# Kernel tuning notes

Hardware: AMD Instinct MI355X
Metric: run time of the kernel (lower is better)

The kernel has to match this reference:

```python
import jax, jax.numpy as jnp
import numpy as np

NZ = 1024       # opts.nz (== NH so layer-0 input weights stack with other layers)
NH = 1024       # opts.nh
NSTATE = 64     # opts.n_state
NLAYERS = 4
MAX_PRIM_LEN = 100
T = MAX_PRIM_LEN + 1   # max_unroll=True runs exactly max_prim_len+1 steps
P_BIAS = 1.0           # opts.dec_p_bias


def setup_inputs() -> dict:
    key = jax.random.key(0)
    ks = jax.random.split(key, 9)
    s_ih = 1.0 / np.sqrt(NH)
    u = lambda k, shape: jax.random.uniform(k, shape, jnp.float32, -s_ih, s_ih)
    return {
        "z": jax.random.normal(ks[0], (1, NZ), jnp.float32),
        # torch LSTM params, gate order (i, f, g, o); layer0 input dim == NZ == NH
        "Wih": u(ks[1], (NLAYERS, 4 * NH, NH)),
        "Whh": u(ks[2], (NLAYERS, 4 * NH, NH)),
        "bih": u(ks[3], (NLAYERS, 4 * NH)),
        "bhh": u(ks[4], (NLAYERS, 4 * NH)),
        "Ws": u(ks[5], (NSTATE, NH)),
        "bs": u(ks[6], (NSTATE,)),
        "Wp": u(ks[7], (2, NH)),
        "bp": u(ks[8], (2,)),
    }


def reference(z, Wih, Whh, bih, bhh, Ws, bs, Wp, bp):
    z0 = z.reshape(-1)  # (NZ,)
    zeros = jnp.zeros_like(z0)

    def step(carry, i):
        h, c = carry                      # each (NLAYERS, NH)
        x = jnp.where(i == 0, z0, zeros)  # input is z at t=0, zeros after
        hs, cs = [], []
        inp = x
        for l in range(NLAYERS):
            gates = Wih[l] @ inp + bih[l] + Whh[l] @ h[l] + bhh[l]
            gi, gf, gg, go = jnp.split(gates, 4)
            cl = jax.nn.sigmoid(gf) * c[l] + jax.nn.sigmoid(gi) * jnp.tanh(gg)
            hl = jax.nn.sigmoid(go) * jnp.tanh(cl)
            hs.append(hl)
            cs.append(cl)
            inp = hl
        o = inp                            # top-layer output, (NH,)
        s = Ws @ o + bs                    # state head, (NSTATE,)
        logits = (Wp @ o + bp).at[0].add(P_BIAS)
        p = jax.nn.softmax(logits)         # (2,)
        last = i == T - 1                  # torch: t > max_prim_len -> force [0,1]
        p = jnp.where(last, jnp.array([0.0, 1.0], p.dtype), p)
        samp = jnp.where(last, 1, 0).astype(jnp.int64)  # max_unroll forces 0 until last
        return (jnp.stack(hs), jnp.stack(cs)), (s, p, samp)

    h0 = jnp.zeros((NLAYERS, NH), z.dtype)
    _, (states, probs, samples) = jax.lax.scan(step, (h0, h0), jnp.arange(T))
    return states[:, None, :], probs[:, None, :], samples[:, None]
```

## Files before the change

### kernel.cpp

```cpp
#include <hip/hip_runtime.h>


#define TT    101
#define NBLK  256
#define NTH   512
#define NREP  8
#define SLAB_U32 512
#define HB16_BYTES (4 * TT * NREP * SLAB_U32 * 4)
#define OUT_PROBS 6464
#define OUT_SAMP  6666
#define SENT 0xFFFFFFFFu

typedef _Float16 h2 __attribute__((ext_vector_type(2)));

__device__ __forceinline__ h2 mkh2(float a, float b) {
    h2 r; r.x = (_Float16)a; r.y = (_Float16)b; return r;
}
__device__ __forceinline__ unsigned pack2(float a, float b) {
    return __builtin_bit_cast(unsigned, mkh2(a, b));
}
__device__ __forceinline__ h2 as_h2(unsigned u) { return __builtin_bit_cast(h2, u); }

#if __has_builtin(__builtin_amdgcn_fdot2)
__device__ __forceinline__ float fdot2(h2 a, h2 b, float c) {
    return __builtin_amdgcn_fdot2(a, b, c, false);
}
#else
__device__ __forceinline__ float fdot2(h2 a, h2 b, float c) {
    return fmaf((float)a.x, (float)b.x, fmaf((float)a.y, (float)b.y, c));
}
#endif

__device__ __forceinline__ uint4 load16_bypass(const uint4* p) {
    uint4 r;
    asm volatile("global_load_dwordx4 %0, %1, off sc0 sc1\n\ts_waitcnt vmcnt(0)"
                 : "=v"(r) : "v"(p) : "memory");
    return r;
}
__device__ __forceinline__ void store4_bypass(unsigned* p, unsigned v) {
    asm volatile("global_store_dword %0, %1, off sc0 sc1" :: "v"(p), "v"(v) : "memory");
}
__device__ __forceinline__ uint4 poll16(const uint4* p) {
    uint4 r = load16_bypass(p);
    while (r.x == SENT || r.y == SENT || r.z == SENT || r.w == SENT) {
        __builtin_amdgcn_s_sleep(1);
        r = load16_bypass(p);
    }
    return r;
}

__device__ __forceinline__ float wave_sum(float x) {
    int v;
    v = __builtin_amdgcn_update_dpp(0, __builtin_bit_cast(int, x), 0x111, 0xf, 0xf, false);
    x += __builtin_bit_cast(float, v);
    v = __builtin_amdgcn_update_dpp(0, __builtin_bit_cast(int, x), 0x112, 0xf, 0xf, false);
    x += __builtin_bit_cast(float, v);
    v = __builtin_amdgcn_update_dpp(0, __builtin_bit_cast(int, x), 0x114, 0xf, 0xe, false);
    x += __builtin_bit_cast(float, v);
    v = __builtin_amdgcn_update_dpp(0, __builtin_bit_cast(int, x), 0x118, 0xf, 0xc, false);
    x += __builtin_bit_cast(float, v);
    v = __builtin_amdgcn_update_dpp(0, __builtin_bit_cast(int, x), 0x142, 0xa, 0xf, false);
    x += __builtin_bit_cast(float, v);
    v = __builtin_amdgcn_update_dpp(0, __builtin_bit_cast(int, x), 0x143, 0xc, 0xf, false);
    x += __builtin_bit_cast(float, v);
    return __builtin_bit_cast(float, __builtin_amdgcn_readlane(__builtin_bit_cast(int, x), 63));
}

__device__ __forceinline__ float sigm(float x) { return 1.f / (1.f + expf(-x)); }

__global__ __launch_bounds__(NTH, 2) void lstm_kernel(
    const float* __restrict__ z,
    const float* __restrict__ Wih, const float* __restrict__ Whh,
    const float* __restrict__ bih, const float* __restrict__ bhh,
    const float* __restrict__ Ws,  const float* __restrict__ bs,
    const float* __restrict__ Wp,  const float* __restrict__ bp,
    unsigned* __restrict__ hb16, float* __restrict__ out)
{
    const int tid  = threadIdx.x;
    const int wv   = tid >> 6;
    const int lane = tid & 63;
    const int l    = blockIdx.x >> 6;
    const int gb   = blockIdx.x & 63;
    const int uA   = (gb << 4) + (wv << 1);

    __shared__ __align__(16) uint4 vh4[256];
    __shared__ unsigned hout[8];

    h2 w[8][16];
    #pragma unroll
    for (int r = 0; r < 8; ++r) {
        const int u = uA + (r >> 2);
        const int g = r & 3;
        const size_t row = ((size_t)((l << 12) + (g << 10) + u)) << 10;
        const float4* pa = (const float4*)(Whh + row + (lane << 3));
        const float4* pb = (const float4*)(Whh + row + 512 + (lane << 3));
        const float4* pc = (const float4*)(Wih + row + (lane << 3));
        const float4* pd = (const float4*)(Wih + row + 512 + (lane << 3));
        float4 f;
        f = pa[0]; w[r][0]  = mkh2(f.x, f.y); w[r][1]  = mkh2(f.z, f.w);
        f = pa[1]; w[r][2]  = mkh2(f.x, f.y); w[r][3]  = mkh2(f.z, f.w);
        f = pb[0]; w[r][4]  = mkh2(f.x, f.y); w[r][5]  = mkh2(f.z, f.w);
        f = pb[1]; w[r][6]  = mkh2(f.x, f.y); w[r][7]  = mkh2(f.z, f.w);
        f = pc[0]; w[r][8]  = mkh2(f.x, f.y); w[r][9]  = mkh2(f.z, f.w);
        f = pc[1]; w[r][10] = mkh2(f.x, f.y); w[r][11] = mkh2(f.z, f.w);
        f = pd[0]; w[r][12] = mkh2(f.x, f.y); w[r][13] = mkh2(f.z, f.w);
        f = pd[1]; w[r][14] = mkh2(f.x, f.y); w[r][15] = mkh2(f.z, f.w);
    }

    float bA[4], bB[4];
    #pragma unroll
    for (int g = 0; g < 4; ++g) {
        const int iA = (l << 12) + (g << 10) + uA;
        bA[g] = bih[iA] + bhh[iA];
        bB[g] = bih[iA + 1] + bhh[iA + 1];
    }

    const bool role_states = (l == 0 && wv == 6);
    const bool role_probs  = (l == 1 && gb == 0 && wv == 6);
    float hw0[16], hw1[16], hb0 = 0.f, hb1 = 0.f;
    if (role_states) {
        #pragma unroll
        for (int k = 0; k < 16; ++k) hw0[k] = Ws[(gb << 10) + (lane << 4) + k];
        hb0 = bs[gb];
    } else if (role_probs) {
        #pragma unroll
        for (int k = 0; k < 16; ++k) {
            hw0[k] = Wp[(lane << 4) + k];
            hw1[k] = Wp[1024 + (lane << 4) + k];
        }
        hb0 = bp[0]; hb1 = bp[1];
    }
    int th = 0;

    float cstA = 0.f, cstB = 0.f;

    #pragma unroll 1
    for (int t = 0; t < TT; ++t) {
        const bool full = (l > 0) || (t == 0);
        const int rep = (gb + wv) & (NREP - 1);

        if (wv < 2) {
            const int c = (wv << 6) + lane;
            if (t == 0) vh4[c] = make_uint4(0, 0, 0, 0);
            else {
                const uint4* slab = (const uint4*)(hb16 + (size_t)((l * TT + t - 1) * NREP + rep) * SLAB_U32);
                vh4[c] = poll16(slab + c);
            }
        } else if (wv < 4) {
            const int c = ((wv - 2) << 6) + lane;
            if (l > 0) {
                const uint4* slab = (const uint4*)(hb16 + (size_t)(((l - 1) * TT + t) * NREP + rep) * SLAB_U32);
                vh4[128 + c] = poll16(slab + c);
            } else if (t == 0) {
                const float4 f0 = *(const float4*)(z + (c << 3));
                const float4 f1 = *(const float4*)(z + (c << 3) + 4);
                vh4[128 + c] = make_uint4(pack2(f0.x, f0.y), pack2(f0.z, f0.w),
                                          pack2(f1.x, f1.y), pack2(f1.z, f1.w));
            }
        }
        __syncthreads();

        float acc[8] = {0.f, 0.f, 0.f, 0.f, 0.f, 0.f, 0.f, 0.f};
        {
            const uint4 A1 = vh4[lane];
            const uint4 A2 = vh4[64 + lane];
            const unsigned a8[8] = {A1.x, A1.y, A1.z, A1.w, A2.x, A2.y, A2.z, A2.w};
            #pragma unroll
            for (int k = 0; k < 8; ++k) {
                const h2 v2 = as_h2(a8[k]);
                #pragma unroll
                for (int r = 0; r < 8; ++r) acc[r] = fdot2(w[r][k], v2, acc[r]);
            }
            if (full) {
                const uint4 B1 = vh4[128 + lane];
                const uint4 B2 = vh4[192 + lane];
                const unsigned b8[8] = {B1.x, B1.y, B1.z, B1.w, B2.x, B2.y, B2.z, B2.w};
                #pragma unroll
                for (int k = 0; k < 8; ++k) {
                    const h2 v2 = as_h2(b8[k]);
                    #pragma unroll
                    for (int r = 0; r < 8; ++r) acc[r] = fdot2(w[r][8 + k], v2, acc[r]);
                }
            }
        }

        float tot[8];
        #pragma unroll
        for (int r = 0; r < 8; ++r) tot[r] = wave_sum(acc[r]);

        cstA = fmaf(sigm(tot[1] + bA[1]), cstA, sigm(tot[0] + bA[0]) * tanhf(tot[2] + bA[2]));
        cstB = fmaf(sigm(tot[5] + bB[1]), cstB, sigm(tot[4] + bB[0]) * tanhf(tot[6] + bB[2]));
        const float hA = sigm(tot[3] + bA[3]) * tanhf(cstA);
        const float hB = sigm(tot[7] + bB[3]) * tanhf(cstB);
        if (lane == 0) hout[wv] = pack2(hA, hB);
        __syncthreads();

        if (wv == 7) {
            const unsigned val = hout[lane & 7];
            unsigned* addr = hb16 + (size_t)(l * TT + t) * NREP * SLAB_U32
                           + (size_t)(lane >> 3) * SLAB_U32 + (gb << 3) + (lane & 7);
            store4_bypass(addr, val);
        } else if ((role_states || role_probs) && th < TT && th <= t - 3) {
            const int hrep = (gb + th) & (NREP - 1);
            const uint4* slab3 = (const uint4*)(hb16 + (size_t)((3 * TT + th) * NREP + hrep) * SLAB_U32);
            const uint4 r0 = load16_bypass(slab3 + (lane << 1));
            const uint4 r1 = load16_bypass(slab3 + (lane << 1) + 1);
            const bool ok = !(r0.x == SENT || r0.y == SENT || r0.z == SENT || r0.w == SENT ||
                              r1.x == SENT || r1.y == SENT || r1.z == SENT || r1.w == SENT);
            if (__ballot(ok) == ~0ull) {
                const unsigned u8[8] = {r0.x, r0.y, r0.z, r0.w, r1.x, r1.y, r1.z, r1.w};
                if (role_states) {
                    float a = 0.f;
                    #pragma unroll
                    for (int j = 0; j < 8; ++j) {
                        const h2 p = as_h2(u8[j]);
                        a = fmaf(hw0[2 * j], (float)p.x, a);
                        a = fmaf(hw0[2 * j + 1], (float)p.y, a);
                    }
                    const float tots = wave_sum(a);
                    if (lane == 0) out[th * 64 + gb] = tots + hb0;
                } else {
                    float a0 = 0.f, a1 = 0.f;
                    #pragma unroll
                    for (int j = 0; j < 8; ++j) {
                        const h2 p = as_h2(u8[j]);
                        a0 = fmaf(hw0[2 * j], (float)p.x, a0); a0 = fmaf(hw0[2 * j + 1], (float)p.y, a0);
                        a1 = fmaf(hw1[2 * j], (float)p.x, a1); a1 = fmaf(hw1[2 * j + 1], (float)p.y, a1);
                    }
                    const float t0 = wave_sum(a0), t1 = wave_sum(a1);
                    if (lane == 0) {
                        float p0, p1;
                        if (th == TT - 1) { p0 = 0.f; p1 = 1.f; }
                        else {
                            const float l0 = t0 + hb0 + 1.0f;
                            const float l1 = t1 + hb1;
                            const float m  = fmaxf(l0, l1);
                            const float e0 = expf(l0 - m), e1 = expf(l1 - m);
                            const float inv = 1.f / (e0 + e1);
                            p0 = e0 * inv; p1 = e1 * inv;
                        }
                        out[OUT_PROBS + 2 * th]     = p0;
                        out[OUT_PROBS + 2 * th + 1] = p1;
                        out[OUT_SAMP + th] = (th == TT - 1) ? 1.0f : 0.0f;
                    }
                }
                ++th;
            }
        }
    }

    if (role_states || role_probs) {
        while (th < TT) {
            const int hrep = (gb + th) & (NREP - 1);
            const uint4* slab3 = (const uint4*)(hb16 + (size_t)((3 * TT + th) * NREP + hrep) * SLAB_U32);
            const uint4 r0 = poll16(slab3 + (lane << 1));
            const uint4 r1 = poll16(slab3 + (lane << 1) + 1);
            const unsigned u8[8] = {r0.x, r0.y, r0.z, r0.w, r1.x, r1.y, r1.z, r1.w};
            if (role_states) {
                float a = 0.f;
                #pragma unroll
                for (int j = 0; j < 8; ++j) {
                    const h2 p = as_h2(u8[j]);
                    a = fmaf(hw0[2 * j], (float)p.x, a);
                    a = fmaf(hw0[2 * j + 1], (float)p.y, a);
                }
                const float tots = wave_sum(a);
                if (lane == 0) out[th * 64 + gb] = tots + hb0;
            } else {
                float a0 = 0.f, a1 = 0.f;
                #pragma unroll
                for (int j = 0; j < 8; ++j) {
                    const h2 p = as_h2(u8[j]);
                    a0 = fmaf(hw0[2 * j], (float)p.x, a0); a0 = fmaf(hw0[2 * j + 1], (float)p.y, a0);
                    a1 = fmaf(hw1[2 * j], (float)p.x, a1); a1 = fmaf(hw1[2 * j + 1], (float)p.y, a1);
                }
                const float t0 = wave_sum(a0), t1 = wave_sum(a1);
                if (lane == 0) {
                    float p0, p1;
                    if (th == TT - 1) { p0 = 0.f; p1 = 1.f; }
                    else {
                        const float l0 = t0 + hb0 + 1.0f;
                        const float l1 = t1 + hb1;
                        const float m  = fmaxf(l0, l1);
                        const float e0 = expf(l0 - m), e1 = expf(l1 - m);
                        const float inv = 1.f / (e0 + e1);
                        p0 = e0 * inv; p1 = e1 * inv;
                    }
                    out[OUT_PROBS + 2 * th]     = p0;
                    out[OUT_PROBS + 2 * th + 1] = p1;
                    out[OUT_SAMP + th] = (th == TT - 1) ? 1.0f : 0.0f;
                }
            }
            ++th;
        }
    }
}

extern "C" void kernel_launch(void* const* d_in, const int* in_sizes, int n_in,
                              void* d_out, int out_size, void* d_ws, size_t ws_size,
                              hipStream_t stream)
{
    const float* z   = (const float*)d_in[0];
    const float* Wih = (const float*)d_in[1];
    const float* Whh = (const float*)d_in[2];
    const float* bih = (const float*)d_in[3];
    const float* bhh = (const float*)d_in[4];
    const float* Ws  = (const float*)d_in[5];
    const float* bs  = (const float*)d_in[6];
    const float* Wp  = (const float*)d_in[7];
    const float* bp  = (const float*)d_in[8];
    float* out = (float*)d_out;

    unsigned* hb16 = (unsigned*)d_ws;

    hipMemsetAsync(hb16, 0xFF, HB16_BYTES, stream);
    lstm_kernel<<<NBLK, NTH, 0, stream>>>(z, Wih, Whh, bih, bhh,
                                          Ws, bs, Wp, bp, hb16, out);
}
```

Measured before the change: 506.2 us.

## Double-buffer LDS vectors, pipeline polling, replace barrier with LDS flag handoff

Double-buffers the shared hidden-state vectors so waves 0-3 fetch the next step's inputs right after the current step's compute, which drops one __syncthreads per step. Wave 7 now waits on sentinel-flagged LDS slots instead of a barrier. Polling uses a hand-written asm loop that keeps two sets of per-dword loads in flight and retires lanes as they complete. Fast __expf-based sigmoid/tanh and paired loads for the head reads are added. The LDS spin handoff and the fast math add correctness and precision risk.

Measured after the change: 573.7 us. 13.3% more time.

```diff
diff --git a/kernel.cpp b/kernel.cpp
--- a/kernel.cpp
+++ b/kernel.cpp
@@ -31,22 +31,88 @@
 }
 #endif
 
-__device__ __forceinline__ uint4 load16_bypass(const uint4* p) {
-    uint4 r;
-    asm volatile("global_load_dwordx4 %0, %1, off sc0 sc1\n\ts_waitcnt vmcnt(0)"
-                 : "=v"(r) : "v"(p) : "memory");
-    return r;
-}
 __device__ __forceinline__ void store4_bypass(unsigned* p, unsigned v) {
     asm volatile("global_store_dword %0, %1, off sc0 sc1" :: "v"(p), "v"(v) : "memory");
 }
-__device__ __forceinline__ uint4 poll16(const uint4* p) {
-    uint4 r = load16_bypass(p);
-    while (r.x == SENT || r.y == SENT || r.z == SENT || r.w == SENT) {
-        __builtin_amdgcn_s_sleep(1);
-        r = load16_bypass(p);
-    }
-    return r;
+
+__device__ __forceinline__ void load32_bypass2(const uint4* p0, const uint4* p1,
+                                               uint4& r0, uint4& r1) {
+    asm volatile("global_load_dwordx4 %0, %2, off sc0 sc1\n\t"
+                 "global_load_dwordx4 %1, %3, off sc0 sc1\n\t"
+                 "s_waitcnt vmcnt(0)"
+                 : "=&v"(r0), "=&v"(r1) : "v"(p0), "v"(p1) : "memory");
+}
+
+__device__ __forceinline__ uint4 poll16_pipe(const uint4* p) {
+    unsigned r0, r1, r2, r3, a0, a1, a2, a3, b0, b1, b2, b3;
+    unsigned long long se, sm, st;
+    asm volatile(
+        "s_mov_b64 %12, exec\n\t"
+        "global_load_dword %4, %15, off sc0 sc1\n\t"
+        "global_load_dword %5, %15, off offset:4 sc0 sc1\n\t"
+        "global_load_dword %6, %15, off offset:8 sc0 sc1\n\t"
+        "global_load_dword %7, %15, off offset:12 sc0 sc1\n\t"
+        "s_sleep 8\n\t"
+        "global_load_dword %8, %15, off sc0 sc1\n\t"
+        "global_load_dword %9, %15, off offset:4 sc0 sc1\n\t"
+        "global_load_dword %10, %15, off offset:8 sc0 sc1\n\t"
+        "global_load_dword %11, %15, off offset:12 sc0 sc1\n\t"
+        "Lploop%=:\n\t"
+        "s_waitcnt vmcnt(4)\n\t"
+        "v_cmp_ne_u32 vcc, -1, %4\n\t"
+        "s_mov_b64 %13, vcc\n\t"
+        "v_cmp_ne_u32 vcc, -1, %5\n\t"
+        "s_and_b64 %13, %13, vcc\n\t"
+        "v_cmp_ne_u32 vcc, -1, %6\n\t"
+        "s_and_b64 %13, %13, vcc\n\t"
+        "v_cmp_ne_u32 vcc, -1, %7\n\t"
+        "s_and_b64 %13, %13, vcc\n\t"
+        "s_mov_b64 %14, exec\n\t"
+        "s_mov_b64 exec, %13\n\t"
+        "v_mov_b32 %0, %4\n\t"
+        "v_mov_b32 %1, %5\n\t"
+        "v_mov_b32 %2, %6\n\t"
+        "v_mov_b32 %3, %7\n\t"
+        "s_mov_b64 exec, %14\n\t"
+        "s_andn2_b64 exec, exec, %13\n\t"
+        "s_cbranch_execz Lpdone%=\n\t"
+        "global_load_dword %4, %15, off sc0 sc1\n\t"
+        "global_load_dword %5, %15, off offset:4 sc0 sc1\n\t"
+        "global_load_dword %6, %15, off offset:8 sc0 sc1\n\t"
+        "global_load_dword %7, %15, off offset:12 sc0 sc1\n\t"
+        "s_waitcnt vmcnt(4)\n\t"
+        "v_cmp_ne_u32 vcc, -1, %8\n\t"
+        "s_mov_b64 %13, vcc\n\t"
+        "v_cmp_ne_u32 vcc, -1, %9\n\t"
+        "s_and_b64 %13, %13, vcc\n\t"
+        "v_cmp_ne_u32 vcc, -1, %10\n\t"
+        "s_and_b64 %13, %13, vcc\n\t"
+        "v_cmp_ne_u32 vcc, -1, %11\n\t"
+        "s_and_b64 %13, %13, vcc\n\t"
+        "s_mov_b64 %14, exec\n\t"
+        "s_mov_b64 exec, %13\n\t"
+        "v_mov_b32 %0, %8\n\t"
+        "v_mov_b32 %1, %9\n\t"
+        "v_mov_b32 %2, %10\n\t"
+        "v_mov_b32 %3, %11\n\t"
+        "s_mov_b64 exec, %14\n\t"
+        "s_andn2_b64 exec, exec, %13\n\t"
+        "s_cbranch_execz Lpdone%=\n\t"
+        "global_load_dword %8, %15, off sc0 sc1\n\t"
+        "global_load_dword %9, %15, off offset:4 sc0 sc1\n\t"
+        "global_load_dword %10, %15, off offset:8 sc0 sc1\n\t"
+        "global_load_dword %11, %15, off offset:12 sc0 sc1\n\t"
+        "s_branch Lploop%=\n\t"
+        "Lpdone%=:\n\t"
+        "s_mov_b64 exec, %12\n\t"
+        "s_waitcnt vmcnt(0)"
+        : "=&v"(r0), "=&v"(r1), "=&v"(r2), "=&v"(r3),
+          "=&v"(a0), "=&v"(a1), "=&v"(a2), "=&v"(a3),
+          "=&v"(b0), "=&v"(b1), "=&v"(b2), "=&v"(b3),
+          "=&s"(se), "=&s"(sm), "=&s"(st)
+        : "v"(p)
+        : "vcc", "scc", "memory");
+    return make_uint4(r0, r1, r2, r3);
 }
 
 __device__ __forceinline__ float wave_sum(float x) {
@@ -66,7 +132,8 @@
     return __builtin_bit_cast(float, __builtin_amdgcn_readlane(__builtin_bit_cast(int, x), 63));
 }
 
-__device__ __forceinline__ float sigm(float x) { return 1.f / (1.f + expf(-x)); }
+__device__ __forceinline__ float sigm(float x)   { return 1.f / (1.f + __expf(-x)); }
+__device__ __forceinline__ float tanh_f(float x) { return 1.f - 2.f / (1.f + __expf(x + x)); }
 
 __global__ __launch_bounds__(NTH, 2) void lstm_kernel(
     const float* __restrict__ z,
@@ -83,7 +150,7 @@
     const int gb   = blockIdx.x & 63;
     const int uA   = (gb << 4) + (wv << 1);
 
-    __shared__ __align__(16) uint4 vh4[256];
+    __shared__ __align__(16) uint4 vh4[2][256];
     __shared__ unsigned hout[8];
 
     h2 w[8][16];
@@ -134,36 +201,34 @@
 
     float cstA = 0.f, cstB = 0.f;
 
+    if (tid < 8) hout[tid] = SENT;
+    if (wv < 2) {
+        const int c = (wv << 6) + lane;
+        vh4[0][c] = make_uint4(0, 0, 0, 0);
+    } else if (wv < 4) {
+        const int c = ((wv - 2) << 6) + lane;
+        if (l == 0) {
+            const float4 f0 = *(const float4*)(z + (c << 3));
+            const float4 f1 = *(const float4*)(z + (c << 3) + 4);
+            vh4[0][128 + c] = make_uint4(pack2(f0.x, f0.y), pack2(f0.z, f0.w),
+                                         pack2(f1.x, f1.y), pack2(f1.z, f1.w));
+        } else {
+            const int rep = (gb + wv) & (NREP - 1);
+            const uint4* slab = (const uint4*)(hb16 + (size_t)(((l - 1) * TT) * NREP + rep) * SLAB_U32);
+            vh4[0][128 + c] = poll16_pipe(slab + c);
+        }
+    }
+    __syncthreads();
+
     #pragma unroll 1
     for (int t = 0; t < TT; ++t) {
         const bool full = (l > 0) || (t == 0);
-        const int rep = (gb + wv) & (NREP - 1);
-
-        if (wv < 2) {
-            const int c = (wv << 6) + lane;
-            if (t == 0) vh4[c] = make_uint4(0, 0, 0, 0);
-            else {
-                const uint4* slab = (const uint4*)(hb16 + (size_t)((l * TT + t - 1) * NREP + rep) * SLAB_U32);
-                vh4[c] = poll16(slab + c);
-            }
-        } else if (wv < 4) {
-            const int c = ((wv - 2) << 6) + lane;
-            if (l > 0) {
-                const uint4* slab = (const uint4*)(hb16 + (size_t)(((l - 1) * TT + t) * NREP + rep) * SLAB_U32);
-                vh4[128 + c] = poll16(slab + c);
-            } else if (t == 0) {
-                const float4 f0 = *(const float4*)(z + (c << 3));
-                const float4 f1 = *(const float4*)(z + (c << 3) + 4);
-                vh4[128 + c] = make_uint4(pack2(f0.x, f0.y), pack2(f0.z, f0.w),
-                                          pack2(f1.x, f1.y), pack2(f1.z, f1.w));
-            }
-        }
-        __syncthreads();
+        const int rb = t & 1;
 
         float acc[8] = {0.f, 0.f, 0.f, 0.f, 0.f, 0.f, 0.f, 0.f};
         {
-            const uint4 A1 = vh4[lane];
-            const uint4 A2 = vh4[64 + lane];
+            const uint4 A1 = vh4[rb][lane];
+            const uint4 A2 = vh4[rb][64 + lane];
             const unsigned a8[8] = {A1.x, A1.y, A1.z, A1.w, A2.x, A2.y, A2.z, A2.w};
             #pragma unroll
             for (int k = 0; k < 8; ++k) {
@@ -172,8 +237,8 @@
                 for (int r = 0; r < 8; ++r) acc[r] = fdot2(w[r][k], v2, acc[r]);
             }
             if (full) {
-                const uint4 B1 = vh4[128 + lane];
-                const uint4 B2 = vh4[192 + lane];
+                const uint4 B1 = vh4[rb][128 + lane];
+                const uint4 B2 = vh4[rb][192 + lane];
                 const unsigned b8[8] = {B1.x, B1.y, B1.z, B1.w, B2.x, B2.y, B2.z, B2.w};
                 #pragma unroll
                 for (int k = 0; k < 8; ++k) {
@@ -188,23 +253,39 @@
         #pragma unroll
         for (int r = 0; r < 8; ++r) tot[r] = wave_sum(acc[r]);
 
-        cstA = fmaf(sigm(tot[1] + bA[1]), cstA, sigm(tot[0] + bA[0]) * tanhf(tot[2] + bA[2]));
-        cstB = fmaf(sigm(tot[5] + bB[1]), cstB, sigm(tot[4] + bB[0]) * tanhf(tot[6] + bB[2]));
-        const float hA = sigm(tot[3] + bA[3]) * tanhf(cstA);
-        const float hB = sigm(tot[7] + bB[3]) * tanhf(cstB);
-        if (lane == 0) hout[wv] = pack2(hA, hB);
-        __syncthreads();
+        cstA = fmaf(sigm(tot[1] + bA[1]), cstA, sigm(tot[0] + bA[0]) * tanh_f(tot[2] + bA[2]));
+        cstB = fmaf(sigm(tot[5] + bB[1]), cstB, sigm(tot[4] + bB[0]) * tanh_f(tot[6] + bB[2]));
+        const float hA = sigm(tot[3] + bA[3]) * tanh_f(cstA);
+        const float hB = sigm(tot[7] + bB[3]) * tanh_f(cstB);
+        if (lane == 0) ((volatile unsigned*)hout)[wv] = pack2(hA, hB);
 
         if (wv == 7) {
-            const unsigned val = hout[lane & 7];
+            volatile unsigned* vho = (volatile unsigned*)hout;
+            unsigned v = vho[lane & 7];
+            while (v == SENT) { v = vho[lane & 7]; }
+            if (lane < 8) vho[lane] = SENT;
             unsigned* addr = hb16 + (size_t)(l * TT + t) * NREP * SLAB_U32
                            + (size_t)(lane >> 3) * SLAB_U32 + (gb << 3) + (lane & 7);
-            store4_bypass(addr, val);
+            store4_bypass(addr, v);
+        } else if (wv < 2) {
+            if (t + 1 < TT) {
+                const int c = (wv << 6) + lane;
+                const int rep = (gb + wv) & (NREP - 1);
+                const uint4* slab = (const uint4*)(hb16 + (size_t)((l * TT + t) * NREP + rep) * SLAB_U32);
+                vh4[rb ^ 1][c] = poll16_pipe(slab + c);
+            }
+        } else if (wv < 4) {
+            if (t + 1 < TT && l > 0) {
+                const int c = ((wv - 2) << 6) + lane;
+                const int rep = (gb + wv) & (NREP - 1);
+                const uint4* slab = (const uint4*)(hb16 + (size_t)(((l - 1) * TT + (t + 1)) * NREP + rep) * SLAB_U32);
+                vh4[rb ^ 1][128 + c] = poll16_pipe(slab + c);
+            }
         } else if ((role_states || role_probs) && th < TT && th <= t - 3) {
             const int hrep = (gb + th) & (NREP - 1);
             const uint4* slab3 = (const uint4*)(hb16 + (size_t)((3 * TT + th) * NREP + hrep) * SLAB_U32);
-            const uint4 r0 = load16_bypass(slab3 + (lane << 1));
-            const uint4 r1 = load16_bypass(slab3 + (lane << 1) + 1);
+            uint4 r0, r1;
+            load32_bypass2(slab3 + (lane << 1), slab3 + (lane << 1) + 1, r0, r1);
             const bool ok = !(r0.x == SENT || r0.y == SENT || r0.z == SENT || r0.w == SENT ||
                               r1.x == SENT || r1.y == SENT || r1.z == SENT || r1.w == SENT);
             if (__ballot(ok) == ~0ull) {
@@ -247,14 +328,20 @@
                 ++th;
             }
         }
+        __syncthreads();
     }
 
     if (role_states || role_probs) {
         while (th < TT) {
             const int hrep = (gb + th) & (NREP - 1);
             const uint4* slab3 = (const uint4*)(hb16 + (size_t)((3 * TT + th) * NREP + hrep) * SLAB_U32);
-            const uint4 r0 = poll16(slab3 + (lane << 1));
-            const uint4 r1 = poll16(slab3 + (lane << 1) + 1);
+            uint4 r0, r1;
+            for (;;) {
+                load32_bypass2(slab3 + (lane << 1), slab3 + (lane << 1) + 1, r0, r1);
+                if (!(r0.x == SENT || r0.y == SENT || r0.z == SENT || r0.w == SENT ||
+                      r1.x == SENT || r1.y == SENT || r1.z == SENT || r1.w == SENT)) break;
+                __builtin_amdgcn_s_sleep(1);
+            }
             const unsigned u8[8] = {r0.x, r0.y, r0.z, r0.w, r1.x, r1.y, r1.z, r1.w};
             if (role_states) {
                 float a = 0.f;
```

## Drop shared-memory staging and block barriers; each wave polls its own hidden state

Applied to the files above, without the earlier changes.

Each wave now loads the previous-step and lower-layer hidden-state slabs from global memory straight into registers, and publishes its own packed h values. This removes the LDS staging buffer and both per-step __syncthreads, so waves within a block no longer wait on each other. The A and B slabs are issued as batched bypass loads behind a single wait. sigmoid and tanh switch to __expf-based approximations. The cost is roughly eight times more global and L2 polling traffic per block, and slightly lower transcendental accuracy.

Result: slower. 1.058 ms (+109.0%).

```diff
diff --git a/kernel.cpp b/kernel.cpp
--- a/kernel.cpp
+++ b/kernel.cpp
@@ -31,22 +31,32 @@
 }
 #endif
 
-__device__ __forceinline__ uint4 load16_bypass(const uint4* p) {
-    uint4 r;
-    asm volatile("global_load_dwordx4 %0, %1, off sc0 sc1\n\ts_waitcnt vmcnt(0)"
-                 : "=v"(r) : "v"(p) : "memory");
-    return r;
-}
 __device__ __forceinline__ void store4_bypass(unsigned* p, unsigned v) {
     asm volatile("global_store_dword %0, %1, off sc0 sc1" :: "v"(p), "v"(v) : "memory");
 }
-__device__ __forceinline__ uint4 poll16(const uint4* p) {
-    uint4 r = load16_bypass(p);
-    while (r.x == SENT || r.y == SENT || r.z == SENT || r.w == SENT) {
-        __builtin_amdgcn_s_sleep(1);
-        r = load16_bypass(p);
-    }
-    return r;
+
+__device__ __forceinline__ void load32_bypass2(const uint4* p0, const uint4* p1,
+                                               uint4& r0, uint4& r1) {
+    asm volatile("global_load_dwordx4 %0, %2, off sc0 sc1\n\t"
+                 "global_load_dwordx4 %1, %3, off sc0 sc1\n\t"
+                 "s_waitcnt vmcnt(0)"
+                 : "=&v"(r0), "=&v"(r1) : "v"(p0), "v"(p1) : "memory");
+}
+
+__device__ __forceinline__ void load64_bypass4(const uint4* p0, const uint4* p1,
+                                               const uint4* p2, const uint4* p3,
+                                               uint4& r0, uint4& r1, uint4& r2, uint4& r3) {
+    asm volatile("global_load_dwordx4 %0, %4, off sc0 sc1\n\t"
+                 "global_load_dwordx4 %1, %5, off sc0 sc1\n\t"
+                 "global_load_dwordx4 %2, %6, off sc0 sc1\n\t"
+                 "global_load_dwordx4 %3, %7, off sc0 sc1\n\t"
+                 "s_waitcnt vmcnt(0)"
+                 : "=&v"(r0), "=&v"(r1), "=&v"(r2), "=&v"(r3)
+                 : "v"(p0), "v"(p1), "v"(p2), "v"(p3) : "memory");
+}
+
+__device__ __forceinline__ bool stale(const uint4& u) {
+    return (u.x == SENT) | (u.y == SENT) | (u.z == SENT) | (u.w == SENT);
 }
 
 __device__ __forceinline__ float wave_sum(float x) {
@@ -66,7 +76,8 @@
     return __builtin_bit_cast(float, __builtin_amdgcn_readlane(__builtin_bit_cast(int, x), 63));
 }
 
-__device__ __forceinline__ float sigm(float x) { return 1.f / (1.f + expf(-x)); }
+__device__ __forceinline__ float sigm(float x)   { return 1.f / (1.f + __expf(-x)); }
+__device__ __forceinline__ float tanh_f(float x) { return 1.f - 2.f / (1.f + __expf(x + x)); }
 
 __global__ __launch_bounds__(NTH, 2) void lstm_kernel(
     const float* __restrict__ z,
@@ -82,9 +93,6 @@
     const int l    = blockIdx.x >> 6;
     const int gb   = blockIdx.x & 63;
     const int uA   = (gb << 4) + (wv << 1);
-
-    __shared__ __align__(16) uint4 vh4[256];
-    __shared__ unsigned hout[8];
 
     h2 w[8][16];
     #pragma unroll
@@ -136,34 +144,53 @@
 
     #pragma unroll 1
     for (int t = 0; t < TT; ++t) {
-        const bool full = (l > 0) || (t == 0);
         const int rep = (gb + wv) & (NREP - 1);
-
-        if (wv < 2) {
-            const int c = (wv << 6) + lane;
-            if (t == 0) vh4[c] = make_uint4(0, 0, 0, 0);
-            else {
-                const uint4* slab = (const uint4*)(hb16 + (size_t)((l * TT + t - 1) * NREP + rep) * SLAB_U32);
-                vh4[c] = poll16(slab + c);
-            }
-        } else if (wv < 4) {
-            const int c = ((wv - 2) << 6) + lane;
-            if (l > 0) {
-                const uint4* slab = (const uint4*)(hb16 + (size_t)(((l - 1) * TT + t) * NREP + rep) * SLAB_U32);
-                vh4[128 + c] = poll16(slab + c);
-            } else if (t == 0) {
-                const float4 f0 = *(const float4*)(z + (c << 3));
-                const float4 f1 = *(const float4*)(z + (c << 3) + 4);
-                vh4[128 + c] = make_uint4(pack2(f0.x, f0.y), pack2(f0.z, f0.w),
-                                          pack2(f1.x, f1.y), pack2(f1.z, f1.w));
-            }
-        }
-        __syncthreads();
+        const bool needA = (t > 0);
+        const bool needB = (l > 0);
+        uint4 A1 = {}, A2 = {}, B1 = {}, B2 = {};
+
+        if (needA && needB) {
+            const uint4* pa = (const uint4*)(hb16 + (size_t)((l * TT + t - 1) * NREP + rep) * SLAB_U32);
+            const uint4* pb = (const uint4*)(hb16 + (size_t)(((l - 1) * TT + t) * NREP + rep) * SLAB_U32);
+            load64_bypass4(pa + lane, pa + 64 + lane, pb + lane, pb + 64 + lane,
+                           A1, A2, B1, B2);
+            while (stale(A1) | stale(A2)) {
+                __builtin_amdgcn_s_sleep(1);
+                load32_bypass2(pa + lane, pa + 64 + lane, A1, A2);
+            }
+            while (stale(B1) | stale(B2)) {
+                __builtin_amdgcn_s_sleep(1);
+                load32_bypass2(pb + lane, pb + 64 + lane, B1, B2);
+            }
+        } else if (needA) {
+            const uint4* pa = (const uint4*)(hb16 + (size_t)((l * TT + t - 1) * NREP + rep) * SLAB_U32);
+            load32_bypass2(pa + lane, pa + 64 + lane, A1, A2);
+            while (stale(A1) | stale(A2)) {
+                __builtin_amdgcn_s_sleep(1);
+                load32_bypass2(pa + lane, pa + 64 + lane, A1, A2);
+            }
+        } else if (needB) {
+            const uint4* pb = (const uint4*)(hb16 + (size_t)(((l - 1) * TT) * NREP + rep) * SLAB_U32);
+            load32_bypass2(pb + lane, pb + 64 + lane, B1, B2);
+            while (stale(B1) | stale(B2)) {
+                __builtin_amdgcn_s_sleep(1);
+                load32_bypass2(pb + lane, pb + 64 + lane, B1, B2);
+            }
+        }
+        const bool fullB = needB || (t == 0);
+        if (l == 0 && t == 0) {
+            const float4 f0 = *(const float4*)(z + (lane << 3));
+            const float4 f1 = *(const float4*)(z + (lane << 3) + 4);
+            const float4 f2 = *(const float4*)(z + 512 + (lane << 3));
+            const float4 f3 = *(const float4*)(z + 512 + (lane << 3) + 4);
+            B1 = make_uint4(pack2(f0.x, f0.y), pack2(f0.z, f0.w),
+                            pack2(f1.x, f1.y), pack2(f1.z, f1.w));
+            B2 = make_uint4(pack2(f2.x, f2.y), pack2(f2.z, f2.w),
+                            pack2(f3.x, f3.y), pack2(f3.z, f3.w));
+        }
 
         float acc[8] = {0.f, 0.f, 0.f, 0.f, 0.f, 0.f, 0.f, 0.f};
-        {
-            const uint4 A1 = vh4[lane];
-            const uint4 A2 = vh4[64 + lane];
+        if (needA) {
             const unsigned a8[8] = {A1.x, A1.y, A1.z, A1.w, A2.x, A2.y, A2.z, A2.w};
             #pragma unroll
             for (int k = 0; k < 8; ++k) {
@@ -171,16 +198,14 @@
                 #pragma unroll
                 for (int r = 0; r < 8; ++r) acc[r] = fdot2(w[r][k], v2, acc[r]);
             }
-            if (full) {
-                const uint4 B1 = vh4[128 + lane];
-                const uint4 B2 = vh4[192 + lane];
-                const unsigned b8[8] = {B1.x, B1.y, B1.z, B1.w, B2.x, B2.y, B2.z, B2.w};
+        }
+        if (fullB) {
+            const unsigned b8[8] = {B1.x, B1.y, B1.z, B1.w, B2.x, B2.y, B2.z, B2.w};
+            #pragma unroll
+            for (int k = 0; k < 8; ++k) {
+                const h2 v2 = as_h2(b8[k]);
                 #pragma unroll
-                for (int k = 0; k < 8; ++k) {
-                    const h2 v2 = as_h2(b8[k]);
-                    #pragma unroll
-                    for (int r = 0; r < 8; ++r) acc[r] = fdot2(w[r][8 + k], v2, acc[r]);
-                }
+                for (int r = 0; r < 8; ++r) acc[r] = fdot2(w[r][8 + k], v2, acc[r]);
             }
         }
 
@@ -188,25 +213,24 @@
         #pragma unroll
         for (int r = 0; r < 8; ++r) tot[r] = wave_sum(acc[r]);
 
-        cstA = fmaf(sigm(tot[1] + bA[1]), cstA, sigm(tot[0] + bA[0]) * tanhf(tot[2] + bA[2]));
-        cstB = fmaf(sigm(tot[5] + bB[1]), cstB, sigm(tot[4] + bB[0]) * tanhf(tot[6] + bB[2]));
-        const float hA = sigm(tot[3] + bA[3]) * tanhf(cstA);
-        const float hB = sigm(tot[7] + bB[3]) * tanhf(cstB);
-        if (lane == 0) hout[wv] = pack2(hA, hB);
-        __syncthreads();
-
-        if (wv == 7) {
-            const unsigned val = hout[lane & 7];
-            unsigned* addr = hb16 + (size_t)(l * TT + t) * NREP * SLAB_U32
-                           + (size_t)(lane >> 3) * SLAB_U32 + (gb << 3) + (lane & 7);
+        cstA = fmaf(sigm(tot[1] + bA[1]), cstA, sigm(tot[0] + bA[0]) * tanh_f(tot[2] + bA[2]));
+        cstB = fmaf(sigm(tot[5] + bB[1]), cstB, sigm(tot[4] + bB[0]) * tanh_f(tot[6] + bB[2]));
+        const float hA = sigm(tot[3] + bA[3]) * tanh_f(cstA);
+        const float hB = sigm(tot[7] + bB[3]) * tanh_f(cstB);
+
+        const unsigned val = pack2(hA, hB);
+        if (lane < NREP) {
+            unsigned* addr = hb16 + (size_t)((l * TT + t) * NREP) * SLAB_U32
+                           + (size_t)lane * SLAB_U32 + (gb << 3) + wv;
             store4_bypass(addr, val);
-        } else if ((role_states || role_probs) && th < TT && th <= t - 3) {
+        }
+
+        if ((role_states || role_probs) && th < TT && th <= t - 3) {
             const int hrep = (gb + th) & (NREP - 1);
             const uint4* slab3 = (const uint4*)(hb16 + (size_t)((3 * TT + th) * NREP + hrep) * SLAB_U32);
-            const uint4 r0 = load16_bypass(slab3 + (lane << 1));
-            const uint4 r1 = load16_bypass(slab3 + (lane << 1) + 1);
-            const bool ok = !(r0.x == SENT || r0.y == SENT || r0.z == SENT || r0.w == SENT ||
-                              r1.x == SENT || r1.y == SENT || r1.z == SENT || r1.w == SENT);
+            uint4 r0, r1;
+            load32_bypass2(slab3 + (lane << 1), slab3 + (lane << 1) + 1, r0, r1);
+            const bool ok = !(stale(r0) | stale(r1));
             if (__ballot(ok) == ~0ull) {
                 const unsigned u8[8] = {r0.x, r0.y, r0.z, r0.w, r1.x, r1.y, r1.z, r1.w};
                 if (role_states) {
@@ -253,8 +277,12 @@
         while (th < TT) {
             const int hrep = (gb + th) & (NREP - 1);
             const uint4* slab3 = (const uint4*)(hb16 + (size_t)((3 * TT + th) * NREP + hrep) * SLAB_U32);
-            const uint4 r0 = poll16(slab3 + (lane << 1));
-            const uint4 r1 = poll16(slab3 + (lane << 1) + 1);
+            uint4 r0, r1;
+            for (;;) {
+                load32_bypass2(slab3 + (lane << 1), slab3 + (lane << 1) + 1, r0, r1);
+                if (!(stale(r0) | stale(r1))) break;
+                __builtin_amdgcn_s_sleep(1);
+            }
             const unsigned u8[8] = {r0.x, r0.y, r0.z, r0.w, r1.x, r1.y, r1.z, r1.w};
             if (role_states) {
                 float a = 0.f;
```

## Gate slab polling on per-step arrival counters and use fast exp activations

Applied to the files above, without the earlier changes.

Adds a per-(layer, step) atomic counter that each producer block bumps after storing its h slice. Consumers whose first slab read is stale now spin on that single counter until all 64 producers have arrived, then re-read the slab. This is meant to cut repeated wide polling traffic on the h buffers. The change also merges the paired 16-byte bypass loads into one asm block with a single wait, and swaps expf/tanhf for __expf-based sigmoid and tanh. The fast math loses some accuracy, and the counter path only runs if the workspace is large enough.

Measured after the change: 644.6 us. 1.27x slower.

```diff
diff --git a/kernel.cpp b/kernel.cpp
--- a/kernel.cpp
+++ b/kernel.cpp
@@ -6,7 +6,9 @@
 #define NTH   512
 #define NREP  8
 #define SLAB_U32 512
-#define HB16_BYTES (4 * TT * NREP * SLAB_U32 * 4)
+#define HB16_U32  (4 * TT * NREP * SLAB_U32)
+#define HB16_BYTES (HB16_U32 * 4)
+#define CNT_BYTES (4 * TT * 4)
 #define OUT_PROBS 6464
 #define OUT_SAMP  6666
 #define SENT 0xFFFFFFFFu
@@ -37,14 +39,38 @@
                  : "=v"(r) : "v"(p) : "memory");
     return r;
 }
+__device__ __forceinline__ unsigned load4_bypass(const unsigned* p) {
+    unsigned r;
+    asm volatile("global_load_dword %0, %1, off sc0 sc1\n\ts_waitcnt vmcnt(0)"
+                 : "=v"(r) : "v"(p) : "memory");
+    return r;
+}
 __device__ __forceinline__ void store4_bypass(unsigned* p, unsigned v) {
     asm volatile("global_store_dword %0, %1, off sc0 sc1" :: "v"(p), "v"(v) : "memory");
 }
-__device__ __forceinline__ uint4 poll16(const uint4* p) {
+__device__ __forceinline__ void load32_bypass2(const uint4* p0, const uint4* p1,
+                                               uint4& r0, uint4& r1) {
+    asm volatile("global_load_dwordx4 %0, %2, off sc0 sc1\n\t"
+                 "global_load_dwordx4 %1, %3, off sc0 sc1\n\t"
+                 "s_waitcnt vmcnt(0)"
+                 : "=&v"(r0), "=&v"(r1) : "v"(p0), "v"(p1) : "memory");
+}
+
+__device__ __forceinline__ bool stale(const uint4& u) {
+    return (u.x == SENT) | (u.y == SENT) | (u.z == SENT) | (u.w == SENT);
+}
+
+__device__ __forceinline__ uint4 poll16_gated(const uint4* p, const unsigned* ca) {
     uint4 r = load16_bypass(p);
-    while (r.x == SENT || r.y == SENT || r.z == SENT || r.w == SENT) {
-        __builtin_amdgcn_s_sleep(1);
+    if (stale(r)) {
+        if (ca) {
+            while (load4_bypass(ca) < 64u) __builtin_amdgcn_s_sleep(2);
+        }
         r = load16_bypass(p);
+        while (stale(r)) {
+            __builtin_amdgcn_s_sleep(1);
+            r = load16_bypass(p);
+        }
     }
     return r;
 }
@@ -66,7 +92,8 @@
     return __builtin_bit_cast(float, __builtin_amdgcn_readlane(__builtin_bit_cast(int, x), 63));
 }
 
-__device__ __forceinline__ float sigm(float x) { return 1.f / (1.f + expf(-x)); }
+__device__ __forceinline__ float sigm(float x)   { return 1.f / (1.f + __expf(-x)); }
+__device__ __forceinline__ float tanh_f(float x) { return 1.f - 2.f / (1.f + __expf(x + x)); }
 
 __global__ __launch_bounds__(NTH, 2) void lstm_kernel(
     const float* __restrict__ z,
@@ -74,7 +101,8 @@
     const float* __restrict__ bih, const float* __restrict__ bhh,
     const float* __restrict__ Ws,  const float* __restrict__ bs,
     const float* __restrict__ Wp,  const float* __restrict__ bp,
-    unsigned* __restrict__ hb16, float* __restrict__ out)
+    unsigned* __restrict__ hb16, unsigned* __restrict__ cnt,
+    float* __restrict__ out)
 {
     const int tid  = threadIdx.x;
     const int wv   = tid >> 6;
@@ -144,13 +172,15 @@
             if (t == 0) vh4[c] = make_uint4(0, 0, 0, 0);
             else {
                 const uint4* slab = (const uint4*)(hb16 + (size_t)((l * TT + t - 1) * NREP + rep) * SLAB_U32);
-                vh4[c] = poll16(slab + c);
+                const unsigned* ca = cnt ? cnt + (l * TT + t - 1) : nullptr;
+                vh4[c] = poll16_gated(slab + c, ca);
             }
         } else if (wv < 4) {
             const int c = ((wv - 2) << 6) + lane;
             if (l > 0) {
                 const uint4* slab = (const uint4*)(hb16 + (size_t)(((l - 1) * TT + t) * NREP + rep) * SLAB_U32);
-                vh4[128 + c] = poll16(slab + c);
+                const unsigned* ca = cnt ? cnt + ((l - 1) * TT + t) : nullptr;
+                vh4[128 + c] = poll16_gated(slab + c, ca);
             } else if (t == 0) {
                 const float4 f0 = *(const float4*)(z + (c << 3));
                 const float4 f1 = *(const float4*)(z + (c << 3) + 4);
@@ -188,10 +218,10 @@
         #pragma unroll
         for (int r = 0; r < 8; ++r) tot[r] = wave_sum(acc[r]);
 
-        cstA = fmaf(sigm(tot[1] + bA[1]), cstA, sigm(tot[0] + bA[0]) * tanhf(tot[2] + bA[2]));
-        cstB = fmaf(sigm(tot[5] + bB[1]), cstB, sigm(tot[4] + bB[0]) * tanhf(tot[6] + bB[2]));
-        const float hA = sigm(tot[3] + bA[3]) * tanhf(cstA);
-        const float hB = sigm(tot[7] + bB[3]) * tanhf(cstB);
+        cstA = fmaf(sigm(tot[1] + bA[1]), cstA, sigm(tot[0] + bA[0]) * tanh_f(tot[2] + bA[2]));
+        cstB = fmaf(sigm(tot[5] + bB[1]), cstB, sigm(tot[4] + bB[0]) * tanh_f(tot[6] + bB[2]));
+        const float hA = sigm(tot[3] + bA[3]) * tanh_f(cstA);
+        const float hB = sigm(tot[7] + bB[3]) * tanh_f(cstB);
         if (lane == 0) hout[wv] = pack2(hA, hB);
         __syncthreads();
 
@@ -200,13 +230,13 @@
             unsigned* addr = hb16 + (size_t)(l * TT + t) * NREP * SLAB_U32
                            + (size_t)(lane >> 3) * SLAB_U32 + (gb << 3) + (lane & 7);
             store4_bypass(addr, val);
+            if (lane == 0 && cnt) atomicAdd(cnt + (l * TT + t), 1u);
         } else if ((role_states || role_probs) && th < TT && th <= t - 3) {
             const int hrep = (gb + th) & (NREP - 1);
             const uint4* slab3 = (const uint4*)(hb16 + (size_t)((3 * TT + th) * NREP + hrep) * SLAB_U32);
-            const uint4 r0 = load16_bypass(slab3 + (lane << 1));
-            const uint4 r1 = load16_bypass(slab3 + (lane << 1) + 1);
-            const bool ok = !(r0.x == SENT || r0.y == SENT || r0.z == SENT || r0.w == SENT ||
-                              r1.x == SENT || r1.y == SENT || r1.z == SENT || r1.w == SENT);
+            uint4 r0, r1;
+            load32_bypass2(slab3 + (lane << 1), slab3 + (lane << 1) + 1, r0, r1);
+            const bool ok = !(stale(r0) | stale(r1));
             if (__ballot(ok) == ~0ull) {
                 const unsigned u8[8] = {r0.x, r0.y, r0.z, r0.w, r1.x, r1.y, r1.z, r1.w};
                 if (role_states) {
@@ -253,8 +283,16 @@
         while (th < TT) {
             const int hrep = (gb + th) & (NREP - 1);
             const uint4* slab3 = (const uint4*)(hb16 + (size_t)((3 * TT + th) * NREP + hrep) * SLAB_U32);
-            const uint4 r0 = poll16(slab3 + (lane << 1));
-            const uint4 r1 = poll16(slab3 + (lane << 1) + 1);
+            if (cnt) {
+                const unsigned* ca = cnt + (3 * TT + th);
+                while (load4_bypass(ca) < 64u) __builtin_amdgcn_s_sleep(2);
+            }
+            uint4 r0, r1;
+            for (;;) {
+                load32_bypass2(slab3 + (lane << 1), slab3 + (lane << 1) + 1, r0, r1);
+                if (!(stale(r0) | stale(r1))) break;
+                __builtin_amdgcn_s_sleep(1);
+            }
             const unsigned u8[8] = {r0.x, r0.y, r0.z, r0.w, r1.x, r1.y, r1.z, r1.w};
             if (role_states) {
                 float a = 0.f;
@@ -312,8 +350,12 @@
     float* out = (float*)d_out;
 
     unsigned* hb16 = (unsigned*)d_ws;
-
+    unsigned* cnt  = nullptr;
+    if (ws_size >= (size_t)HB16_BYTES + CNT_BYTES) {
+        cnt = hb16 + HB16_U32;
+        hipMemsetAsync(cnt, 0, CNT_BYTES, stream);
+    }
     hipMemsetAsync(hb16, 0xFF, HB16_BYTES, stream);
     lstm_kernel<<<NBLK, NTH, 0, stream>>>(z, Wih, Whh, bih, bhh,
-                                          Ws, bs, Wp, bp, hb16, out);
-}
+                                          Ws, bs, Wp, bp, hb16, cnt, out);
+}
```
